# Performance work log

Hardware: AMD Instinct MI355X
Metric: run time of the kernel (lower is better)

Reference implementation:

```python
import jax, jax.numpy as jnp
import numpy as np

P, B, L = 32, 64, 128
E, HB, HP = 64, 128, 128   # byte emb dim, byte GRU hidden, packet GRU hidden
PE = 2 * HB                # packet embedding dim = 256
LH = 128                   # attention linear hidden
NC = 10                    # num classes


def _gru_dir(x, w_ih, w_hh, b_ih, b_hh, reverse=False):
    # x: [T, N, E_in] -> outputs [T, N, H]; PyTorch GRU gate math, h0 = 0.
    H = w_hh.shape[1]
    xg = jnp.einsum('tne,ge->tng', x, w_ih) + b_ih  # precompute input gates [T,N,3H]
    if reverse:
        xg = xg[::-1]

    def step(h, xgt):
        hg = h @ w_hh.T + b_hh
        xr, xz, xn = jnp.split(xgt, 3, axis=-1)
        hr, hz, hn = jnp.split(hg, 3, axis=-1)
        r = jax.nn.sigmoid(xr + hr)
        z = jax.nn.sigmoid(xz + hz)
        n = jnp.tanh(xn + r * hn)
        h = (1.0 - z) * n + z * h
        return h, h

    h0 = jnp.zeros((x.shape[1], H), x.dtype)
    _, ys = jax.lax.scan(step, h0, xg)
    if reverse:
        ys = ys[::-1]
    return ys


def _bigru(x, wif, whf, bif, bhf, wib, whb, bib, bhb):
    f = _gru_dir(x, wif, whf, bif, bhf, reverse=False)
    b = _gru_dir(x, wib, whb, bib, bhb, reverse=True)
    return jnp.concatenate([f, b], axis=-1)


def setup_inputs() -> dict:
    key = jax.random.key(0)
    ks = jax.random.split(key, 32)
    rn = lambda k, shp: (jax.random.normal(k, shp, dtype=jnp.float32) * 0.05)
    inp = {}
    inp['flow'] = jax.random.randint(ks[0], (P, B, L), 0, 256, dtype=jnp.int64)
    inp['emb'] = rn(ks[1], (256, E))
    # byte biGRU (forward / backward dirs)
    inp['byte_wih_f'] = rn(ks[2], (3 * HB, E)); inp['byte_whh_f'] = rn(ks[3], (3 * HB, HB))
    inp['byte_bih_f'] = rn(ks[4], (3 * HB,));   inp['byte_bhh_f'] = rn(ks[5], (3 * HB,))
    inp['byte_wih_b'] = rn(ks[6], (3 * HB, E)); inp['byte_whh_b'] = rn(ks[7], (3 * HB, HB))
    inp['byte_bih_b'] = rn(ks[8], (3 * HB,));   inp['byte_bhh_b'] = rn(ks[9], (3 * HB,))
    # packet biGRU
    inp['pkt_wih_f'] = rn(ks[10], (3 * HP, PE)); inp['pkt_whh_f'] = rn(ks[11], (3 * HP, HP))
    inp['pkt_bih_f'] = rn(ks[12], (3 * HP,));    inp['pkt_bhh_f'] = rn(ks[13], (3 * HP,))
    inp['pkt_wih_b'] = rn(ks[14], (3 * HP, PE)); inp['pkt_whh_b'] = rn(ks[15], (3 * HP, HP))
    inp['pkt_bih_b'] = rn(ks[16], (3 * HP,));    inp['pkt_bhh_b'] = rn(ks[17], (3 * HP,))
    # byte attention (Linear(2HB->LH), Linear(LH->1))
    inp['ba_w1'] = rn(ks[18], (LH, 2 * HB)); inp['ba_b1'] = rn(ks[19], (LH,))
    inp['ba_w2'] = rn(ks[20], (1, LH));      inp['ba_b2'] = rn(ks[21], (1,))
    # packet attention (Linear(2HP->LH), Linear(LH->1))
    inp['pa_w1'] = rn(ks[22], (LH, 2 * HP)); inp['pa_b1'] = rn(ks[23], (LH,))
    inp['pa_w2'] = rn(ks[24], (1, LH));      inp['pa_b2'] = rn(ks[25], (1,))
    # final classifier
    inp['wf'] = rn(ks[26], (NC, 2 * HP)); inp['bf'] = rn(ks[27], (NC,))
    return inp


def reference(flow, emb,
              byte_wih_f, byte_whh_f, byte_bih_f, byte_bhh_f,
              byte_wih_b, byte_whh_b, byte_bih_b, byte_bhh_b,
              pkt_wih_f, pkt_whh_f, pkt_bih_f, pkt_bhh_f,
              pkt_wih_b, pkt_whh_b, pkt_bih_b, pkt_bhh_b,
              ba_w1, ba_b1, ba_w2, ba_b2,
              pa_w1, pa_b1, pa_w2, pa_b2,
              wf, bf):
    p, b, l = flow.shape
    x = emb[flow]                                   # [P,B,L,E]
    # batch the per-packet byte GRU across packets: [L, P*B, E]
    xb = x.transpose(2, 0, 1, 3).reshape(l, p * b, E)
    out = _bigru(xb, byte_wih_f, byte_whh_f, byte_bih_f, byte_bhh_f,
                 byte_wih_b, byte_whh_b, byte_bih_b, byte_bhh_b)  # [L, P*B, 2HB]
    out = out.reshape(l, p, b, 2 * HB)
    # Attention: tanh(lin1) -> lin2 -> softmax over dim=1 of the [L,B,1] view,
    # i.e. over the batch axis (faithful to the original code).
    h = jnp.tanh(jnp.einsum('lpbd,hd->lpbh', out, ba_w1) + ba_b1)
    score = jnp.einsum('lpbh,oh->lpbo', h, ba_w2) + ba_b2          # [L,P,B,1]
    attn = jax.nn.softmax(score, axis=2)
    packet_emb = (out * attn).sum(axis=0)                          # [P,B,2HB]
    # packet biGRU over packet sequence
    out2 = _bigru(packet_emb, pkt_wih_f, pkt_whh_f, pkt_bih_f, pkt_bhh_f,
                  pkt_wih_b, pkt_whh_b, pkt_bih_b, pkt_bhh_b)      # [P,B,2HP]
    h2 = jnp.tanh(jnp.einsum('pbd,hd->pbh', out2, pa_w1) + pa_b1)
    score2 = jnp.einsum('pbh,oh->pbo', h2, pa_w2) + pa_b2          # [P,B,1]
    attn2 = jax.nn.softmax(score2, axis=1)
    flow_emb = (out2 * attn2).sum(axis=1)                          # [P,2HP] (faithful sum over dim=1)
    return flow_emb @ wf.T + bf                                    # [P,NC]
```

## Files before the change

kernel.cpp:

```cpp
#include <hip/hip_runtime.h>
#include <hip/hip_bf16.h>
#include <hip/hip_fp16.h>
#include <cstdint>
#include <cstddef>


#define DINLINE __device__ __forceinline__

typedef _Float16 f16;
typedef f16 f16x8 __attribute__((ext_vector_type(8)));
typedef float f32x4 __attribute__((ext_vector_type(4)));

static DINLINE float fast_sigmoid(float x) {
    const float e = __builtin_amdgcn_exp2f(-1.44269504089f * x);
    return __builtin_amdgcn_rcpf(1.0f + e);
}
static DINLINE float fast_tanh(float x) {
    const float e = __builtin_amdgcn_exp2f(2.88539008178f * x);
    return 1.0f - 2.0f * __builtin_amdgcn_rcpf(1.0f + e);
}

__global__ void k_tables(const float* __restrict__ emb,
                         const float* __restrict__ wihF, const float* __restrict__ bihF,
                         const float* __restrict__ bhhF,
                         const float* __restrict__ wihB, const float* __restrict__ bihB,
                         const float* __restrict__ bhhB,
                         float* __restrict__ tabF, float* __restrict__ tabB) {
    const int v = blockIdx.x & 255;
    const int dir = blockIdx.x >> 8;
    const float* wih = dir ? wihB : wihF;
    const float* bih = dir ? bihB : bihF;
    const float* bhh = dir ? bhhB : bhhF;
    float* tab = dir ? tabB : tabF;
    __shared__ float er[64];
    if (threadIdx.x < 64) er[threadIdx.x] = emb[v * 64 + threadIdx.x];
    __syncthreads();
    const int g = threadIdx.x;
    float acc = bih[g] + (g < 256 ? bhh[g] : 0.0f);
    #pragma unroll
    for (int e = 0; e < 64; ++e) acc = fmaf(wih[g * 64 + e], er[e], acc);
    tab[v * 384 + g] = acc;
}

struct TransArgs {
    const float* src[2];
    float* dst[2];
    int R[2];
    int C[2];
};
__global__ void k_transpose(TransArgs a) {
    const int m = blockIdx.y;
    const float* __restrict__ s = a.src[m];
    float* __restrict__ d = a.dst[m];
    const int R = a.R[m], C = a.C[m];
    const int total = R * C;
    for (int idx = blockIdx.x * blockDim.x + threadIdx.x; idx < total;
         idx += gridDim.x * blockDim.x) {
        const int r = idx / C, c = idx - r * C;
        d[c * R + r] = s[idx];
    }
}

__global__ __launch_bounds__(512, 1) void k_byte_gru(
    const int* __restrict__ flow,
    const float* __restrict__ tabF, const float* __restrict__ tabB,
    const float* __restrict__ whhF, const float* __restrict__ whhB,
    const float* __restrict__ bhhF, const float* __restrict__ bhhB,
    __half* __restrict__ hF, __half* __restrict__ hB) {
    const int dir = blockIdx.x & 1;
    const int chunk = blockIdx.x >> 1;
    const int row0 = chunk * 16;
    const int tid = threadIdx.x;
    const int wid = tid >> 6;
    const int lane = tid & 63;
    const int c = lane & 15;
    const int q = lane >> 4;
    const int j = wid * 16 + c;

    const float* __restrict__ tab = dir ? tabB : tabF;
    const float* __restrict__ whh = dir ? whhB : whhF;
    const float* __restrict__ bhh = dir ? bhhB : bhhF;
    __half* __restrict__ hout = dir ? hB : hF;

    __shared__ f16 hbuf[2][16 * 128];
    __shared__ int flow_lds[16][128];

    for (int i = tid; i < 16 * 128; i += 512)
        flow_lds[i >> 7][i & 127] = flow[row0 * 128 + i] & 255;
    for (int i = tid; i < 16 * 128; i += 512) hbuf[0][i] = (f16)0.f;

    f16x8 Bf[3][4];
    #pragma unroll
    for (int g = 0; g < 3; ++g) {
        #pragma unroll
        for (int ks = 0; ks < 4; ++ks) {
            const float* src = whh + (size_t)(g * 128 + j) * 128 + ks * 32 + q * 8;
            f16x8 b;
            #pragma unroll
            for (int e = 0; e < 8; ++e) b[e] = (f16)src[e];
            Bf[g][ks] = b;
        }
    }
    const float bh2 = bhh[j + 256];
    float hold[4];
    #pragma unroll
    for (int rr = 0; rr < 4; ++rr) hold[rr] = 0.f;
    __syncthreads();

    for (int t = 0; t < 128; ++t) {
        const int curb = t & 1, nxtb = curb ^ 1;
        const int tt = dir ? (127 - t) : t;

        int byt[4];
        #pragma unroll
        for (int rr = 0; rr < 4; ++rr) byt[rr] = flow_lds[q * 4 + rr][tt];
        float xr[4], xz[4], xn[4];
        #pragma unroll
        for (int rr = 0; rr < 4; ++rr) {
            const float* tb = tab + byt[rr] * 384 + j;
            xr[rr] = tb[0];
            xz[rr] = tb[128];
            xn[rr] = tb[256];
        }

        f16x8 Af[4];
        #pragma unroll
        for (int ks = 0; ks < 4; ++ks) {
            const int kb = ks * 32 + q * 8;
            const int idx = c * 128 + (kb ^ ((c & 7) << 3));
            Af[ks] = *reinterpret_cast<const f16x8*>(&hbuf[curb][idx]);
        }

        f32x4 a0 = {0.f, 0.f, 0.f, 0.f};
        f32x4 a1 = {0.f, 0.f, 0.f, 0.f};
        f32x4 a2 = {0.f, 0.f, 0.f, 0.f};
        #pragma unroll
        for (int ks = 0; ks < 4; ++ks) {
            a0 = __builtin_amdgcn_mfma_f32_16x16x32_f16(Af[ks], Bf[0][ks], a0, 0, 0, 0);
            a1 = __builtin_amdgcn_mfma_f32_16x16x32_f16(Af[ks], Bf[1][ks], a1, 0, 0, 0);
            a2 = __builtin_amdgcn_mfma_f32_16x16x32_f16(Af[ks], Bf[2][ks], a2, 0, 0, 0);
        }

        #pragma unroll
        for (int rr = 0; rr < 4; ++rr) {
            const float rg = fast_sigmoid(xr[rr] + a0[rr]);
            const float zg = fast_sigmoid(xz[rr] + a1[rr]);
            const float ng = fast_tanh(xn[rr] + rg * (a2[rr] + bh2));
            const float hn = fmaf(zg, hold[rr] - ng, ng);
            hold[rr] = hn;
            const int row = q * 4 + rr;
            hbuf[nxtb][row * 128 + (j ^ ((row & 7) << 3))] = (f16)hn;
        }
        __syncthreads();

        {
            const int row = tid >> 5;
            const int ho = (tid & 31) * 4;
            const int idx = row * 128 + (ho ^ ((row & 7) << 3));
            const uint2 v = *reinterpret_cast<const uint2*>(&hbuf[nxtb][idx]);
            *reinterpret_cast<uint2*>(
                &hout[((size_t)tt * 2048 + row0 + row) * 128 + ho]) = v;
        }
    }
}

__global__ __launch_bounds__(256, 1) void k_scores_attn(
    const __half* __restrict__ hF, const __half* __restrict__ hB,
    const float* __restrict__ w1,
    const float* __restrict__ b1, const float* __restrict__ w2,
    const float* __restrict__ b2, float* __restrict__ attn) {
    __shared__ f16 w1lds[128 * 256];
    __shared__ float sc[128];
    const int tid = threadIdx.x;
    for (int i = tid; i < 128 * 256; i += 256) {
        const int col = i >> 8, k = i & 255;
        w1lds[col * 256 + (k ^ ((col & 7) << 3))] = (f16)w1[i];
    }
    const int lane = tid & 63, w = tid >> 6;
    const int c = lane & 15, q = lane >> 4;
    const int pos0 = blockIdx.x * 128;

    f16x8 Af[2][8];
    #pragma unroll
    for (int pt = 0; pt < 2; ++pt) {
        const size_t pos = (size_t)pos0 + (w * 2 + pt) * 16 + c;
        const f16* hFp = (const f16*)(hF + pos * 128);
        const f16* hBp = (const f16*)(hB + pos * 128);
        #pragma unroll
        for (int ks = 0; ks < 4; ++ks)
            Af[pt][ks] = *reinterpret_cast<const f16x8*>(hFp + ks * 32 + q * 8);
        #pragma unroll
        for (int ks = 0; ks < 4; ++ks)
            Af[pt][4 + ks] = *reinterpret_cast<const f16x8*>(hBp + ks * 32 + q * 8);
    }

    float b1v[8], w2v[8];
    #pragma unroll
    for (int ct = 0; ct < 8; ++ct) {
        b1v[ct] = b1[ct * 16 + c];
        w2v[ct] = w2[ct * 16 + c];
    }
    const float b2v = b2[0];
    __syncthreads();

    float s[2][4] = {{0.f, 0.f, 0.f, 0.f}, {0.f, 0.f, 0.f, 0.f}};
    #pragma unroll
    for (int ct = 0; ct < 8; ++ct) {
        const int jj = ct * 16 + c;
        f16x8 Bfr[8];
        #pragma unroll
        for (int ks = 0; ks < 8; ++ks) {
            const int k = ks * 32 + q * 8;
            Bfr[ks] = *reinterpret_cast<const f16x8*>(
                &w1lds[jj * 256 + (k ^ ((jj & 7) << 3))]);
        }
        #pragma unroll
        for (int pt = 0; pt < 2; ++pt) {
            f32x4 acc = {0.f, 0.f, 0.f, 0.f};
            #pragma unroll
            for (int ks = 0; ks < 8; ++ks)
                acc = __builtin_amdgcn_mfma_f32_16x16x32_f16(Af[pt][ks], Bfr[ks],
                                                             acc, 0, 0, 0);
            #pragma unroll
            for (int rr = 0; rr < 4; ++rr)
                s[pt][rr] += w2v[ct] * fast_tanh(acc[rr] + b1v[ct]);
        }
    }
    #pragma unroll
    for (int pt = 0; pt < 2; ++pt) {
        #pragma unroll
        for (int rr = 0; rr < 4; ++rr) {
            float v = s[pt][rr];
            v += __shfl_xor(v, 1);
            v += __shfl_xor(v, 2);
            v += __shfl_xor(v, 4);
            v += __shfl_xor(v, 8);
            if (c == 0) sc[(w * 2 + pt) * 16 + q * 4 + rr] = v + b2v;
        }
    }
    __syncthreads();
    if (tid < 128) {
        const float sv = sc[tid];
        float m = sv;
        for (int off = 32; off; off >>= 1) m = fmaxf(m, __shfl_xor(m, off));
        const float e = __expf(sv - m);
        float sum = e;
        for (int off = 32; off; off >>= 1) sum += __shfl_xor(sum, off);
        attn[pos0 + tid] = e / sum;
    }
}

__global__ __launch_bounds__(256) void k_packet_emb(
    const __half* __restrict__ hF, const __half* __restrict__ hB,
    const float* __restrict__ attn, float* __restrict__ pe) {
    const int tid = threadIdx.x;
    const int g = tid >> 6;
    const int lane = tid & 63;
    const int n = blockIdx.x * 4 + g;
    const bool isF = lane < 32;
    const int chunk = lane & 31;
    const __half* __restrict__ hsrc = (isF ? hF : hB) + (size_t)n * 128 + chunk * 4;
    float acc0 = 0.f, acc1 = 0.f, acc2 = 0.f, acc3 = 0.f;
    #pragma unroll 4
    for (int l = 0; l < 128; ++l) {
        const float wv = attn[l * 2048 + n];
        const uint2 u = *reinterpret_cast<const uint2*>(hsrc + (size_t)l * 2048 * 128);
        const f16* hv = reinterpret_cast<const f16*>(&u);
        acc0 = fmaf(wv, (float)hv[0], acc0);
        acc1 = fmaf(wv, (float)hv[1], acc1);
        acc2 = fmaf(wv, (float)hv[2], acc2);
        acc3 = fmaf(wv, (float)hv[3], acc3);
    }
    float4 o = {acc0, acc1, acc2, acc3};
    *reinterpret_cast<float4*>(&pe[n * 256 + (isF ? 0 : 128) + chunk * 4]) = o;
}

__global__ __launch_bounds__(384) void k_pkt_xg(
    const float* __restrict__ pe, const float* __restrict__ wihTF,
    const float* __restrict__ bihF, const float* __restrict__ bhhF,
    const float* __restrict__ wihTB, const float* __restrict__ bihB,
    const float* __restrict__ bhhB, float* __restrict__ xgF,
    float* __restrict__ xgB) {
    const int dir = blockIdx.y;
    const float* __restrict__ wihT = dir ? wihTB : wihTF;
    const float* __restrict__ bih = dir ? bihB : bihF;
    const float* __restrict__ bhh = dir ? bhhB : bhhF;
    float* __restrict__ xg = dir ? xgB : xgF;
    const int rbase = blockIdx.x * 8;
    __shared__ float xrow[8][256];
    for (int i = threadIdx.x; i < 8 * 256; i += 384)
        xrow[i >> 8][i & 255] = pe[rbase * 256 + i];
    __syncthreads();
    const int g = threadIdx.x;
    float acc[8];
    const float bias = bih[g] + (g < 256 ? bhh[g] : 0.0f);
    #pragma unroll
    for (int r = 0; r < 8; ++r) acc[r] = bias;
    for (int d = 0; d < 256; ++d) {
        const float w = wihT[d * 384 + g];
        #pragma unroll
        for (int r = 0; r < 8; ++r) acc[r] = fmaf(w, xrow[r][d], acc[r]);
    }
    #pragma unroll
    for (int r = 0; r < 8; ++r) xg[(rbase + r) * 384 + g] = acc[r];
}

__global__ __launch_bounds__(512, 1) void k_pkt_gru(
    const float* __restrict__ xgF, const float* __restrict__ xgB,
    const float* __restrict__ whhF, const float* __restrict__ whhB,
    const float* __restrict__ bhhF, const float* __restrict__ bhhB,
    float* __restrict__ h2F, float* __restrict__ h2B) {
    const int dir = blockIdx.x & 1;
    const int chunk = blockIdx.x >> 1;
    const int row0 = chunk * 16;
    const int tid = threadIdx.x;
    const int wid = tid >> 6;
    const int lane = tid & 63;
    const int c = lane & 15;
    const int q = lane >> 4;
    const int j = wid * 16 + c;

    const float* __restrict__ xg = dir ? xgB : xgF;
    const float* __restrict__ whh = dir ? whhB : whhF;
    const float* __restrict__ bhh = dir ? bhhB : bhhF;
    float* __restrict__ hout = dir ? h2B : h2F;

    __shared__ f16 hbuf[2][16 * 128];

    for (int i = tid; i < 16 * 128; i += 512) hbuf[0][i] = (f16)0.f;

    f16x8 Bf[3][4];
    #pragma unroll
    for (int g = 0; g < 3; ++g) {
        #pragma unroll
        for (int ks = 0; ks < 4; ++ks) {
            const float* src = whh + (size_t)(g * 128 + j) * 128 + ks * 32 + q * 8;
            f16x8 b;
            #pragma unroll
            for (int e = 0; e < 8; ++e) b[e] = (f16)src[e];
            Bf[g][ks] = b;
        }
    }
    const float bh2 = bhh[j + 256];
    float hold[4];
    #pragma unroll
    for (int rr = 0; rr < 4; ++rr) hold[rr] = 0.f;
    __syncthreads();

    for (int t = 0; t < 32; ++t) {
        const int curb = t & 1, nxtb = curb ^ 1;
        const int tt = dir ? (31 - t) : t;

        float xr[4], xz[4], xn[4];
        #pragma unroll
        for (int rr = 0; rr < 4; ++rr) {
            const float* xp = xg + ((size_t)tt * 64 + row0 + q * 4 + rr) * 384 + j;
            xr[rr] = xp[0];
            xz[rr] = xp[128];
            xn[rr] = xp[256];
        }

        f16x8 Af[4];
        #pragma unroll
        for (int ks = 0; ks < 4; ++ks) {
            const int kb = ks * 32 + q * 8;
            const int idx = c * 128 + (kb ^ ((c & 7) << 3));
            Af[ks] = *reinterpret_cast<const f16x8*>(&hbuf[curb][idx]);
        }

        f32x4 a0 = {0.f, 0.f, 0.f, 0.f};
        f32x4 a1 = {0.f, 0.f, 0.f, 0.f};
        f32x4 a2 = {0.f, 0.f, 0.f, 0.f};
        #pragma unroll
        for (int ks = 0; ks < 4; ++ks) {
            a0 = __builtin_amdgcn_mfma_f32_16x16x32_f16(Af[ks], Bf[0][ks], a0, 0, 0, 0);
            a1 = __builtin_amdgcn_mfma_f32_16x16x32_f16(Af[ks], Bf[1][ks], a1, 0, 0, 0);
            a2 = __builtin_amdgcn_mfma_f32_16x16x32_f16(Af[ks], Bf[2][ks], a2, 0, 0, 0);
        }

        #pragma unroll
        for (int rr = 0; rr < 4; ++rr) {
            const float rg = fast_sigmoid(xr[rr] + a0[rr]);
            const float zg = fast_sigmoid(xz[rr] + a1[rr]);
            const float ng = fast_tanh(xn[rr] + rg * (a2[rr] + bh2));
            const float hn = fmaf(zg, hold[rr] - ng, ng);
            hold[rr] = hn;
            const int row = q * 4 + rr;
            hbuf[nxtb][row * 128 + (j ^ ((row & 7) << 3))] = (f16)hn;
            hout[((size_t)tt * 64 + row0 + row) * 128 + j] = hn;
        }
        __syncthreads();
    }
}

__global__ __launch_bounds__(128) void k_scores2(
    const float* __restrict__ h2F, const float* __restrict__ h2B,
    const float* __restrict__ paw1,
    const float* __restrict__ pab1, const float* __restrict__ paw2,
    const float* __restrict__ pab2, float* __restrict__ scores2) {
    const int n = blockIdx.x;
    const int tid = threadIdx.x;
    __shared__ float x[256];
    __shared__ float red[2];
    x[tid] = h2F[n * 128 + tid];
    x[tid + 128] = h2B[n * 128 + tid];
    __syncthreads();
    float acc = pab1[tid];
    const float* wr = paw1 + tid * 256;
    #pragma unroll 8
    for (int d = 0; d < 256; ++d) acc = fmaf(wr[d], x[d], acc);
    float s = paw2[tid] * fast_tanh(acc);
    s += __shfl_xor(s, 1);
    s += __shfl_xor(s, 2);
    s += __shfl_xor(s, 4);
    s += __shfl_xor(s, 8);
    s += __shfl_xor(s, 16);
    s += __shfl_xor(s, 32);
    if ((tid & 63) == 0) red[tid >> 6] = s;
    __syncthreads();
    if (tid == 0) scores2[n] = red[0] + red[1] + pab2[0];
}

__global__ __launch_bounds__(256) void k_final3(
    const float* __restrict__ h2F, const float* __restrict__ h2B,
    const float* __restrict__ scores2, const float* __restrict__ wf,
    const float* __restrict__ bfv, float* __restrict__ outp) {
    const int p = blockIdx.x;
    const int tid = threadIdx.x;
    __shared__ float sc[64];
    __shared__ float femb[256];
    __shared__ float red[64];

    if (tid < 64) {
        const float s = scores2[p * 64 + tid];
        float m = s;
        for (int off = 32; off; off >>= 1) m = fmaxf(m, __shfl_xor(m, off));
        const float e = __expf(s - m);
        float sum = e;
        for (int off = 32; off; off >>= 1) sum += __shfl_xor(sum, off);
        sc[tid] = e / sum;
    }
    __syncthreads();

    {
        const float* __restrict__ hsrc = (tid < 128) ? h2F : h2B;
        const int d = tid & 127;
        float acc = 0.f;
        for (int b = 0; b < 64; ++b)
            acc = fmaf(sc[b], hsrc[(p * 64 + b) * 128 + d], acc);
        femb[tid] = acc;
    }
    __syncthreads();

    const float fv = femb[tid];
    #pragma unroll
    for (int c = 0; c < 10; ++c) {
        float s = fv * wf[c * 256 + tid];
        s += __shfl_xor(s, 1);
        s += __shfl_xor(s, 2);
        s += __shfl_xor(s, 4);
        s += __shfl_xor(s, 8);
        s += __shfl_xor(s, 16);
        s += __shfl_xor(s, 32);
        if ((tid & 63) == 0) red[(c << 2) | (tid >> 6)] = s;
        __syncthreads();
        if (tid == 0)
            outp[p * 10 + c] = bfv[c] + red[c << 2] + red[(c << 2) | 1] +
                               red[(c << 2) | 2] + red[(c << 2) | 3];
        __syncthreads();
    }
}

extern "C" void kernel_launch(void* const* d_in, const int* in_sizes, int n_in,
                              void* d_out, int out_size, void* d_ws,
                              size_t ws_size, hipStream_t stream) {
    const int* flow = (const int*)d_in[0];
    const float* emb = (const float*)d_in[1];
    const float* byte_wih_f = (const float*)d_in[2];
    const float* byte_whh_f = (const float*)d_in[3];
    const float* byte_bih_f = (const float*)d_in[4];
    const float* byte_bhh_f = (const float*)d_in[5];
    const float* byte_wih_b = (const float*)d_in[6];
    const float* byte_whh_b = (const float*)d_in[7];
    const float* byte_bih_b = (const float*)d_in[8];
    const float* byte_bhh_b = (const float*)d_in[9];
    const float* pkt_wih_f = (const float*)d_in[10];
    const float* pkt_whh_f = (const float*)d_in[11];
    const float* pkt_bih_f = (const float*)d_in[12];
    const float* pkt_bhh_f = (const float*)d_in[13];
    const float* pkt_wih_b = (const float*)d_in[14];
    const float* pkt_whh_b = (const float*)d_in[15];
    const float* pkt_bih_b = (const float*)d_in[16];
    const float* pkt_bhh_b = (const float*)d_in[17];
    const float* ba_w1 = (const float*)d_in[18];
    const float* ba_b1 = (const float*)d_in[19];
    const float* ba_w2 = (const float*)d_in[20];
    const float* ba_b2 = (const float*)d_in[21];
    const float* pa_w1 = (const float*)d_in[22];
    const float* pa_b1 = (const float*)d_in[23];
    const float* pa_w2 = (const float*)d_in[24];
    const float* pa_b2 = (const float*)d_in[25];
    const float* wf = (const float*)d_in[26];
    const float* bf = (const float*)d_in[27];

    char* base = (char*)d_ws;
    size_t off = 0;
    auto allocf = [&](size_t nf) -> float* {
        float* p = (float*)(base + off);
        off += nf * sizeof(float);
        return p;
    };
    auto alloch = [&](size_t nh) -> __half* {
        off = (off + 255) & ~(size_t)255;
        __half* p = (__half*)(base + off);
        off += nh * sizeof(__half);
        return p;
    };
    float* tabF = allocf(256 * 384);
    float* tabB = allocf(256 * 384);
    float* wihTpF = allocf(256 * 384);
    float* wihTpB = allocf(256 * 384);
    float* attn = allocf(262144);
    float* pe = allocf(2048 * 256);
    float* xgF = allocf(32 * 64 * 384);
    float* xgB = allocf(32 * 64 * 384);
    float* h2F = allocf(32 * 64 * 128);
    float* h2B = allocf(32 * 64 * 128);
    float* scores2 = allocf(2048);
    __half* hF = alloch((size_t)128 * 2048 * 128);
    __half* hB = alloch((size_t)128 * 2048 * 128);
    if (off > ws_size) return;
    (void)in_sizes; (void)n_in; (void)out_size;

    k_tables<<<512, 384, 0, stream>>>(emb, byte_wih_f, byte_bih_f, byte_bhh_f,
                                      byte_wih_b, byte_bih_b, byte_bhh_b, tabF,
                                      tabB);

    TransArgs ta;
    ta.src[0] = pkt_wih_f; ta.dst[0] = wihTpF; ta.R[0] = 384; ta.C[0] = 256;
    ta.src[1] = pkt_wih_b; ta.dst[1] = wihTpB; ta.R[1] = 384; ta.C[1] = 256;
    k_transpose<<<dim3(96, 2), 256, 0, stream>>>(ta);

    k_byte_gru<<<256, 512, 0, stream>>>(flow, tabF, tabB, byte_whh_f,
                                        byte_whh_b, byte_bhh_f, byte_bhh_b, hF,
                                        hB);

    k_scores_attn<<<2048, 256, 0, stream>>>(hF, hB, ba_w1, ba_b1, ba_w2, ba_b2,
                                            attn);
    k_packet_emb<<<512, 256, 0, stream>>>(hF, hB, attn, pe);

    k_pkt_xg<<<dim3(256, 2), 384, 0, stream>>>(pe, wihTpF, pkt_bih_f,
                                               pkt_bhh_f, wihTpB, pkt_bih_b,
                                               pkt_bhh_b, xgF, xgB);
    k_pkt_gru<<<8, 512, 0, stream>>>(xgF, xgB, pkt_whh_f, pkt_whh_b,
                                     pkt_bhh_f, pkt_bhh_b, h2F, h2B);
    k_scores2<<<2048, 128, 0, stream>>>(h2F, h2B, pa_w1, pa_b1, pa_w2, pa_b2,
                                        scores2);
    k_final3<<<32, 256, 0, stream>>>(h2F, h2B, scores2, wf, bf, (float*)d_out);
}
```

Baseline: 315.6 us.

## Pack byte-GRU gate tables to fp16, prefetch next step, amortize attention weight load

```diff
diff --git a/kernel.cpp b/kernel.cpp
--- a/kernel.cpp
+++ b/kernel.cpp
@@ -20,26 +20,41 @@
     return 1.0f - 2.0f * __builtin_amdgcn_rcpf(1.0f + e);
 }
 
+static DINLINE void lds_barrier() {
+    asm volatile("s_waitcnt lgkmcnt(0)\n\ts_barrier" ::: "memory");
+}
+
 __global__ void k_tables(const float* __restrict__ emb,
                          const float* __restrict__ wihF, const float* __restrict__ bihF,
                          const float* __restrict__ bhhF,
                          const float* __restrict__ wihB, const float* __restrict__ bihB,
                          const float* __restrict__ bhhB,
-                         float* __restrict__ tabF, float* __restrict__ tabB) {
+                         __half* __restrict__ tab4F, __half* __restrict__ tab4B) {
     const int v = blockIdx.x & 255;
     const int dir = blockIdx.x >> 8;
     const float* wih = dir ? wihB : wihF;
     const float* bih = dir ? bihB : bihF;
     const float* bhh = dir ? bhhB : bhhF;
-    float* tab = dir ? tabB : tabF;
+    __half* tab4 = dir ? tab4B : tab4F;
     __shared__ float er[64];
+    __shared__ float sh[384];
     if (threadIdx.x < 64) er[threadIdx.x] = emb[v * 64 + threadIdx.x];
     __syncthreads();
     const int g = threadIdx.x;
     float acc = bih[g] + (g < 256 ? bhh[g] : 0.0f);
     #pragma unroll
     for (int e = 0; e < 64; ++e) acc = fmaf(wih[g * 64 + e], er[e], acc);
-    tab[v * 384 + g] = acc;
+    sh[g] = acc;
+    __syncthreads();
+    if (g < 128) {
+        f16 pk[4];
+        pk[0] = (f16)sh[g];
+        pk[1] = (f16)sh[g + 128];
+        pk[2] = (f16)sh[g + 256];
+        pk[3] = (f16)0.f;
+        *reinterpret_cast<uint2*>(&tab4[(v * 128 + g) * 4]) =
+            *reinterpret_cast<const uint2*>(pk);
+    }
 }
 
 struct TransArgs {
@@ -63,7 +78,7 @@
 
 __global__ __launch_bounds__(512, 1) void k_byte_gru(
     const int* __restrict__ flow,
-    const float* __restrict__ tabF, const float* __restrict__ tabB,
+    const __half* __restrict__ tab4F, const __half* __restrict__ tab4B,
     const float* __restrict__ whhF, const float* __restrict__ whhB,
     const float* __restrict__ bhhF, const float* __restrict__ bhhB,
     __half* __restrict__ hF, __half* __restrict__ hB) {
@@ -77,7 +92,8 @@
     const int q = lane >> 4;
     const int j = wid * 16 + c;
 
-    const float* __restrict__ tab = dir ? tabB : tabF;
+    const uint2* __restrict__ t4 =
+        reinterpret_cast<const uint2*>(dir ? tab4B : tab4F);
     const float* __restrict__ whh = dir ? whhB : whhF;
     const float* __restrict__ bhh = dir ? bhhB : bhhF;
     __half* __restrict__ hout = dir ? hB : hF;
@@ -107,21 +123,18 @@
     for (int rr = 0; rr < 4; ++rr) hold[rr] = 0.f;
     __syncthreads();
 
+    uint2 xg[4];
+    {
+        const int tt0 = dir ? 127 : 0;
+        #pragma unroll
+        for (int rr = 0; rr < 4; ++rr)
+            xg[rr] = t4[flow_lds[q * 4 + rr][tt0] * 128 + j];
+    }
+
+    #pragma unroll 2
     for (int t = 0; t < 128; ++t) {
         const int curb = t & 1, nxtb = curb ^ 1;
         const int tt = dir ? (127 - t) : t;
-
-        int byt[4];
-        #pragma unroll
-        for (int rr = 0; rr < 4; ++rr) byt[rr] = flow_lds[q * 4 + rr][tt];
-        float xr[4], xz[4], xn[4];
-        #pragma unroll
-        for (int rr = 0; rr < 4; ++rr) {
-            const float* tb = tab + byt[rr] * 384 + j;
-            xr[rr] = tb[0];
-            xz[rr] = tb[128];
-            xn[rr] = tb[256];
-        }
 
         f16x8 Af[4];
         #pragma unroll
@@ -131,6 +144,14 @@
             Af[ks] = *reinterpret_cast<const f16x8*>(&hbuf[curb][idx]);
         }
 
+        uint2 xgn[4];
+        if (t < 127) {
+            const int ttn = dir ? (126 - t) : (t + 1);
+            #pragma unroll
+            for (int rr = 0; rr < 4; ++rr)
+                xgn[rr] = t4[flow_lds[q * 4 + rr][ttn] * 128 + j];
+        }
+
         f32x4 a0 = {0.f, 0.f, 0.f, 0.f};
         f32x4 a1 = {0.f, 0.f, 0.f, 0.f};
         f32x4 a2 = {0.f, 0.f, 0.f, 0.f};
@@ -143,24 +164,19 @@
 
         #pragma unroll
         for (int rr = 0; rr < 4; ++rr) {
-            const float rg = fast_sigmoid(xr[rr] + a0[rr]);
-            const float zg = fast_sigmoid(xz[rr] + a1[rr]);
-            const float ng = fast_tanh(xn[rr] + rg * (a2[rr] + bh2));
+            const f16* xp = reinterpret_cast<const f16*>(&xg[rr]);
+            const float rg = fast_sigmoid((float)xp[0] + a0[rr]);
+            const float zg = fast_sigmoid((float)xp[1] + a1[rr]);
+            const float ng = fast_tanh((float)xp[2] + rg * (a2[rr] + bh2));
             const float hn = fmaf(zg, hold[rr] - ng, ng);
             hold[rr] = hn;
             const int row = q * 4 + rr;
             hbuf[nxtb][row * 128 + (j ^ ((row & 7) << 3))] = (f16)hn;
-        }
-        __syncthreads();
-
-        {
-            const int row = tid >> 5;
-            const int ho = (tid & 31) * 4;
-            const int idx = row * 128 + (ho ^ ((row & 7) << 3));
-            const uint2 v = *reinterpret_cast<const uint2*>(&hbuf[nxtb][idx]);
-            *reinterpret_cast<uint2*>(
-                &hout[((size_t)tt * 2048 + row0 + row) * 128 + ho]) = v;
-        }
+            hout[((size_t)tt * 2048 + row0 + row) * 128 + j] = (__half)hn;
+        }
+        lds_barrier();
+        #pragma unroll
+        for (int rr = 0; rr < 4; ++rr) xg[rr] = xgn[rr];
     }
 }
 
@@ -178,21 +194,6 @@
     }
     const int lane = tid & 63, w = tid >> 6;
     const int c = lane & 15, q = lane >> 4;
-    const int pos0 = blockIdx.x * 128;
-
-    f16x8 Af[2][8];
-    #pragma unroll
-    for (int pt = 0; pt < 2; ++pt) {
-        const size_t pos = (size_t)pos0 + (w * 2 + pt) * 16 + c;
-        const f16* hFp = (const f16*)(hF + pos * 128);
-        const f16* hBp = (const f16*)(hB + pos * 128);
-        #pragma unroll
-        for (int ks = 0; ks < 4; ++ks)
-            Af[pt][ks] = *reinterpret_cast<const f16x8*>(hFp + ks * 32 + q * 8);
-        #pragma unroll
-        for (int ks = 0; ks < 4; ++ks)
-            Af[pt][4 + ks] = *reinterpret_cast<const f16x8*>(hBp + ks * 32 + q * 8);
-    }
 
     float b1v[8], w2v[8];
     #pragma unroll
@@ -203,50 +204,70 @@
     const float b2v = b2[0];
     __syncthreads();
 
-    float s[2][4] = {{0.f, 0.f, 0.f, 0.f}, {0.f, 0.f, 0.f, 0.f}};
-    #pragma unroll
-    for (int ct = 0; ct < 8; ++ct) {
-        const int jj = ct * 16 + c;
-        f16x8 Bfr[8];
-        #pragma unroll
-        for (int ks = 0; ks < 8; ++ks) {
-            const int k = ks * 32 + q * 8;
-            Bfr[ks] = *reinterpret_cast<const f16x8*>(
-                &w1lds[jj * 256 + (k ^ ((jj & 7) << 3))]);
-        }
+    for (int it = 0; it < 4; ++it) {
+        const int pos0 = blockIdx.x * 512 + it * 128;
+
+        f16x8 Af[2][8];
         #pragma unroll
         for (int pt = 0; pt < 2; ++pt) {
-            f32x4 acc = {0.f, 0.f, 0.f, 0.f};
-            #pragma unroll
-            for (int ks = 0; ks < 8; ++ks)
-                acc = __builtin_amdgcn_mfma_f32_16x16x32_f16(Af[pt][ks], Bfr[ks],
-                                                             acc, 0, 0, 0);
-            #pragma unroll
-            for (int rr = 0; rr < 4; ++rr)
-                s[pt][rr] += w2v[ct] * fast_tanh(acc[rr] + b1v[ct]);
-        }
-    }
-    #pragma unroll
-    for (int pt = 0; pt < 2; ++pt) {
-        #pragma unroll
-        for (int rr = 0; rr < 4; ++rr) {
-            float v = s[pt][rr];
-            v += __shfl_xor(v, 1);
-            v += __shfl_xor(v, 2);
-            v += __shfl_xor(v, 4);
-            v += __shfl_xor(v, 8);
-            if (c == 0) sc[(w * 2 + pt) * 16 + q * 4 + rr] = v + b2v;
-        }
-    }
-    __syncthreads();
-    if (tid < 128) {
-        const float sv = sc[tid];
-        float m = sv;
-        for (int off = 32; off; off >>= 1) m = fmaxf(m, __shfl_xor(m, off));
-        const float e = __expf(sv - m);
-        float sum = e;
-        for (int off = 32; off; off >>= 1) sum += __shfl_xor(sum, off);
-        attn[pos0 + tid] = e / sum;
+            const size_t pos = (size_t)pos0 + (w * 2 + pt) * 16 + c;
+            const f16* hFp = (const f16*)(hF + pos * 128);
+            const f16* hBp = (const f16*)(hB + pos * 128);
+            #pragma unroll
+            for (int ks = 0; ks < 4; ++ks)
+                Af[pt][ks] = *reinterpret_cast<const f16x8*>(hFp + ks * 32 + q * 8);
+            #pragma unroll
+            for (int ks = 0; ks < 4; ++ks)
+                Af[pt][4 + ks] = *reinterpret_cast<const f16x8*>(hBp + ks * 32 + q * 8);
+        }
+
+        float s[2][4] = {{0.f, 0.f, 0.f, 0.f}, {0.f, 0.f, 0.f, 0.f}};
+        #pragma unroll
+        for (int ct = 0; ct < 8; ++ct) {
+            const int jj = ct * 16 + c;
+            f16x8 Bfr[8];
+            #pragma unroll
+            for (int ks = 0; ks < 8; ++ks) {
+                const int k = ks * 32 + q * 8;
+                Bfr[ks] = *reinterpret_cast<const f16x8*>(
+                    &w1lds[jj * 256 + (k ^ ((jj & 7) << 3))]);
+            }
+            #pragma unroll
+            for (int pt = 0; pt < 2; ++pt) {
+                f32x4 acc = {0.f, 0.f, 0.f, 0.f};
+                #pragma unroll
+                for (int ks = 0; ks < 8; ++ks)
+                    acc = __builtin_amdgcn_mfma_f32_16x16x32_f16(Af[pt][ks],
+                                                                 Bfr[ks], acc,
+                                                                 0, 0, 0);
+                #pragma unroll
+                for (int rr = 0; rr < 4; ++rr)
+                    s[pt][rr] += w2v[ct] * fast_tanh(acc[rr] + b1v[ct]);
+            }
+        }
+        #pragma unroll
+        for (int pt = 0; pt < 2; ++pt) {
+            #pragma unroll
+            for (int rr = 0; rr < 4; ++rr) {
+                float v = s[pt][rr];
+                v += __shfl_xor(v, 1);
+                v += __shfl_xor(v, 2);
+                v += __shfl_xor(v, 4);
+                v += __shfl_xor(v, 8);
+                if (c == 0) sc[(w * 2 + pt) * 16 + q * 4 + rr] = v + b2v;
+            }
+        }
+        __syncthreads();
+        if (tid < 128) {
+            const float sv = sc[tid];
+            float m = sv;
+            for (int off = 32; off; off >>= 1) m = fmaxf(m, __shfl_xor(m, off));
+            const float e = __expf(sv - m);
+            float sum = e;
+            for (int off = 32; off; off >>= 1) sum += __shfl_xor(sum, off);
+            attn[pos0 + tid] = e / sum;
+        }
+        __syncthreads();
     }
 }
 
@@ -389,7 +410,7 @@
             hbuf[nxtb][row * 128 + (j ^ ((row & 7) << 3))] = (f16)hn;
             hout[((size_t)tt * 64 + row0 + row) * 128 + j] = hn;
         }
-        __syncthreads();
+        lds_barrier();
     }
 }
 
@@ -516,8 +537,6 @@
         off += nh * sizeof(__half);
         return p;
     };
-    float* tabF = allocf(256 * 384);
-    float* tabB = allocf(256 * 384);
     float* wihTpF = allocf(256 * 384);
     float* wihTpB = allocf(256 * 384);
     float* attn = allocf(262144);
@@ -527,26 +546,28 @@
     float* h2F = allocf(32 * 64 * 128);
     float* h2B = allocf(32 * 64 * 128);
     float* scores2 = allocf(2048);
+    __half* tab4F = alloch(256 * 128 * 4);
+    __half* tab4B = alloch(256 * 128 * 4);
     __half* hF = alloch((size_t)128 * 2048 * 128);
     __half* hB = alloch((size_t)128 * 2048 * 128);
     if (off > ws_size) return;
     (void)in_sizes; (void)n_in; (void)out_size;
 
     k_tables<<<512, 384, 0, stream>>>(emb, byte_wih_f, byte_bih_f, byte_bhh_f,
-                                      byte_wih_b, byte_bih_b, byte_bhh_b, tabF,
-                                      tabB);
+                                      byte_wih_b, byte_bih_b, byte_bhh_b,
+                                      tab4F, tab4B);
 
     TransArgs ta;
     ta.src[0] = pkt_wih_f; ta.dst[0] = wihTpF; ta.R[0] = 384; ta.C[0] = 256;
     ta.src[1] = pkt_wih_b; ta.dst[1] = wihTpB; ta.R[1] = 384; ta.C[1] = 256;
     k_transpose<<<dim3(96, 2), 256, 0, stream>>>(ta);
 
-    k_byte_gru<<<256, 512, 0, stream>>>(flow, tabF, tabB, byte_whh_f,
+    k_byte_gru<<<256, 512, 0, stream>>>(flow, tab4F, tab4B, byte_whh_f,
                                         byte_whh_b, byte_bhh_f, byte_bhh_b, hF,
                                         hB);
 
-    k_scores_attn<<<2048, 256, 0, stream>>>(hF, hB, ba_w1, ba_b1, ba_w2, ba_b2,
-                                            attn);
+    k_scores_attn<<<512, 256, 0, stream>>>(hF, hB, ba_w1, ba_b1, ba_w2, ba_b2,
+                                           attn);
     k_packet_emb<<<512, 256, 0, stream>>>(hF, hB, attn, pe);
 
     k_pkt_xg<<<dim3(256, 2), 384, 0, stream>>>(pe, wihTpF, pkt_bih_f,
```

Result: slower. 322.2 us (+2.1%).
